# Optimization experiments

Hardware: AMD Instinct MI355X
Metric: run time of the kernel (lower is better)

Reference implementation:

```python
import jax, jax.numpy as jnp
import numpy as np

XS, YS = 512, 512  # xsize+1, ysize+1 with init args 511, 511


def _grid_sample_align_corners(img, gx, gy):
    """Bilinear grid_sample with align_corners=True, zeros padding.
    img: [C, H, W]; gx, gy: [X, Y] normalized coords in grid_sample convention
    (gx indexes W, gy indexes H). Returns [C, X, Y]."""
    C, H, W = img.shape
    x = (gx + 1.0) * 0.5 * (W - 1)
    y = (gy + 1.0) * 0.5 * (H - 1)
    x0 = jnp.floor(x)
    y0 = jnp.floor(y)
    wx1 = x - x0
    wy1 = y - y0
    out = jnp.zeros((C,) + gx.shape, img.dtype)
    for dy in (0, 1):
        for dx in (0, 1):
            xi = x0 + dx
            yi = y0 + dy
            w = (wx1 if dx else 1.0 - wx1) * (wy1 if dy else 1.0 - wy1)
            valid = (xi >= 0) & (xi <= W - 1) & (yi >= 0) & (yi <= H - 1)
            xc = jnp.clip(xi, 0, W - 1).astype(jnp.int32)
            yc = jnp.clip(yi, 0, H - 1).astype(jnp.int32)
            v = img[:, yc, xc]  # [C, X, Y]
            out = out + v * (w * valid.astype(img.dtype))[None]
    return out


def _per_batch(a, b, c, pnts, coors, contain):
    # a/b/c: [C,H,W] feature maps; pnts: [P,2] in [0,1]; coors: [P,3] int; contain: [P] int
    keep = contain > 0
    # route invalid pillars to an out-of-bounds index -> dropped by scatter
    cx = jnp.where(keep, coors[:, 1], XS)
    cy = jnp.where(keep, coors[:, 2], YS)
    grid = jnp.full((XS, YS, 2), -2.0, a.dtype)
    grid = grid.at[cx, cy, :].set(pnts * 2.0 - 1.0, mode='drop')
    mask = jnp.zeros((XS, YS), a.dtype).at[cx, cy].set(1.0, mode='drop')
    gx, gy = grid[..., 0], grid[..., 1]
    fa = _grid_sample_align_corners(a, gx, gy) * mask[None]
    fb = _grid_sample_align_corners(b, gx, gy) * mask[None]
    fc = _grid_sample_align_corners(c, gx, gy) * mask[None]
    return fa, fb, fc


def reference(c3, c4, c5, dynamic_img, pillar_img_pts, rgb_coors, contains_rgb):
    fa, fb, fc = jax.vmap(_per_batch)(c3, c4, c5, pillar_img_pts, rgb_coors, contains_rgb)
    # weighted fusion of the three scales, weights broadcast over channel dim
    return (fa * dynamic_img[:, 0:1]
            + fb * dynamic_img[:, 1:2]
            + fc * dynamic_img[:, 2:3])


def setup_inputs() -> dict:
    key = jax.random.key(0)
    ks = jax.random.split(key, 7)
    B, C, P = 4, 64, 20000
    c3 = jax.random.normal(ks[0], (B, C, 48, 160), jnp.float32)
    c4 = jax.random.normal(ks[1], (B, C, 24, 80), jnp.float32)
    c5 = jax.random.normal(ks[2], (B, C, 12, 40), jnp.float32)
    dynamic_img = jax.random.uniform(ks[3], (B, 3, XS, YS), jnp.float32)
    pillar_img_pts = jax.random.uniform(ks[4], (B, P, 2), jnp.float32)
    rgb_coors = jax.random.randint(ks[5], (B, P, 3), 0, 512, jnp.int32)
    contains_rgb = jax.random.randint(ks[6], (B, P), 0, 2, jnp.int32)
    return {"c3": c3, "c4": c4, "c5": c5, "dynamic_img": dynamic_img,
            "pillar_img_pts": pillar_img_pts, "rgb_coors": rgb_coors,
            "contains_rgb": contains_rgb}
```

## Files before the change

### kernel.cpp

```cpp
#include <hip/hip_runtime.h>
#include <cstddef>

#define XSZ 512
#define YSZ 512
#define NB  4
#define NC  64
#define NP  20000
#define H3 48
#define W3 160
#define H4 24
#define W4 80
#define H5 12
#define W5 40
#define HW3 (H3*W3)
#define HW4 (H4*W4)
#define HW5 (H5*W5)

#define FILL_BLOCKS 256
#define T3_TILES (NB * ((HW3 + 63) / 64))
#define T4_TILES (NB * ((HW4 + 63) / 64))
#define T5_TILES (NB * ((HW5 + 63) / 64))

__global__ void __launch_bounds__(256)
k_init(int4* __restrict__ winner4,
       const float* __restrict__ c3, const float* __restrict__ c4,
       const float* __restrict__ c5,
       float* __restrict__ c3t, float* __restrict__ c4t, float* __restrict__ c5t) {
    int blk = blockIdx.x;
    if (blk < FILL_BLOCKS) {
        int base = blk * 1024 + threadIdx.x;
        int4 m1 = make_int4(-1, -1, -1, -1);
        winner4[base      ] = m1;
        winner4[base + 256] = m1;
        winner4[base + 512] = m1;
        winner4[base + 768] = m1;
        return;
    }
    __shared__ float lds[NC * 65];
    int t = blk - FILL_BLOCKS;
    const float* in; float* outp; int HW, tpb;
    if (t < T3_TILES)                      { in = c3; outp = c3t; HW = HW3; tpb = 120; }
    else if ((t -= T3_TILES) < T4_TILES)   { in = c4; outp = c4t; HW = HW4; tpb = 30; }
    else { t -= T4_TILES;                    in = c5; outp = c5t; HW = HW5; tpb = 8; }
    int b  = t / tpb;
    int p0 = (t - b * tpb) * 64;
    int lane = threadIdx.x & 63, wave = threadIdx.x >> 6;
    const float* in_b  = in   + (size_t)b * NC * HW;
    float*       out_b = outp + (size_t)b * HW * NC;

    int p = p0 + lane;
    if (p < HW) {
        for (int ch = wave; ch < NC; ch += 4)
            lds[ch * 65 + lane] = in_b[(size_t)ch * HW + p];
    }
    __syncthreads();
    for (int pp = wave; pp < 64; pp += 4) {
        int pq = p0 + pp;
        if (pq < HW) out_b[(size_t)pq * NC + lane] = lds[lane * 65 + pp];
    }
}

__global__ void __launch_bounds__(256)
k_scatter(const int* __restrict__ coors, const int* __restrict__ contains,
          int* __restrict__ winner) {
    int idx = blockIdx.x * blockDim.x + threadIdx.x;
    if (idx >= NB * NP) return;
    if (contains[idx] <= 0) return;
    int b  = idx / NP;
    int p  = idx - b * NP;
    int cx = coors[idx * 3 + 1];
    int cy = coors[idx * 3 + 2];
    if ((unsigned)cx >= XSZ || (unsigned)cy >= YSZ) return;
    atomicMax(&winner[((size_t)b * XSZ + cx) * YSZ + cy], p);
}

__device__ __forceinline__ float bilinT(const float* __restrict__ img, int H, int W,
                                        float px, float py, int c) {
    float gx = px * 2.0f - 1.0f;
    float gy = py * 2.0f - 1.0f;
    float x = (gx + 1.0f) * 0.5f * (float)(W - 1);
    float y = (gy + 1.0f) * 0.5f * (float)(H - 1);
    float x0f = floorf(x), y0f = floorf(y);
    float wx1 = x - x0f,   wy1 = y - y0f;
    float wx0 = 1.0f - wx1, wy0 = 1.0f - wy1;
    int x0 = (int)x0f, y0 = (int)y0f;
    float acc = 0.0f;
#pragma unroll
    for (int dy = 0; dy < 2; ++dy) {
#pragma unroll
        for (int dx = 0; dx < 2; ++dx) {
            int xi = x0 + dx, yi = y0 + dy;
            bool valid = (xi >= 0) && (xi <= W - 1) && (yi >= 0) && (yi <= H - 1);
            int xc = min(max(xi, 0), W - 1);
            int yc = min(max(yi, 0), H - 1);
            float w = (dx ? wx1 : wx0) * (dy ? wy1 : wy0);
            float v = img[(size_t)(yc * W + xc) * NC + c];
            acc = fmaf(v, valid ? w : 0.0f, acc);
        }
    }
    return acc;
}

__device__ __forceinline__ float bilinG(const float* __restrict__ img, int H, int W,
                                        float px, float py, int c, int sChan) {
    float gx = px * 2.0f - 1.0f;
    float gy = py * 2.0f - 1.0f;
    float x = (gx + 1.0f) * 0.5f * (float)(W - 1);
    float y = (gy + 1.0f) * 0.5f * (float)(H - 1);
    float x0f = floorf(x), y0f = floorf(y);
    float wx1 = x - x0f,   wy1 = y - y0f;
    float wx0 = 1.0f - wx1, wy0 = 1.0f - wy1;
    int x0 = (int)x0f, y0 = (int)y0f;
    float acc = 0.0f;
#pragma unroll
    for (int dy = 0; dy < 2; ++dy) {
#pragma unroll
        for (int dx = 0; dx < 2; ++dx) {
            int xi = x0 + dx, yi = y0 + dy;
            bool valid = (xi >= 0) && (xi <= W - 1) && (yi >= 0) && (yi <= H - 1);
            int xc = min(max(xi, 0), W - 1);
            int yc = min(max(yi, 0), H - 1);
            float w = (dx ? wx1 : wx0) * (dy ? wy1 : wy0);
            float v = img[(size_t)(yc * W + xc) + (size_t)c * sChan];
            acc = fmaf(v, valid ? w : 0.0f, acc);
        }
    }
    return acc;
}

__global__ void __launch_bounds__(256)
k_samp(const int* __restrict__ coors, const int* __restrict__ contains,
       const float* __restrict__ pnts, const int* __restrict__ winner,
       const float* __restrict__ i3t, const float* __restrict__ i4t,
       const float* __restrict__ i5t, const float* __restrict__ dyn,
       float* __restrict__ cvals) {
    int nw   = gridDim.x << 2;
    int wv   = (blockIdx.x << 2) + (threadIdx.x >> 6);
    int lane = threadIdx.x & 63;
    for (int idx = wv; idx < NB * NP; idx += nw) {
        if (contains[idx] <= 0) continue;
        int b = idx / NP;
        int p = idx - b * NP;
        int cx = coors[idx * 3 + 1];
        int cy = coors[idx * 3 + 2];
        if ((unsigned)cx >= XSZ || (unsigned)cy >= YSZ) continue;
        if (winner[((size_t)b * XSZ + cx) * YSZ + cy] != p) continue;
        float px = pnts[idx * 2], py = pnts[idx * 2 + 1];
        float fa = bilinT(i3t + (size_t)b * HW3 * NC, H3, W3, px, py, lane);
        float fb = bilinT(i4t + (size_t)b * HW4 * NC, H4, W4, px, py, lane);
        float fc = bilinT(i5t + (size_t)b * HW5 * NC, H5, W5, px, py, lane);
        size_t dbase = (((size_t)b * 3) * XSZ + cx) * YSZ + cy;
        float d0 = dyn[dbase];
        float d1 = dyn[dbase + (size_t)XSZ * YSZ];
        float d2 = dyn[dbase + (size_t)2 * XSZ * YSZ];
        cvals[(size_t)idx * NC + lane] = fa * d0 + fb * d1 + fc * d2;
    }
}

__global__ void __launch_bounds__(256)
k_samp_fb(const int* __restrict__ coors, const int* __restrict__ contains,
          const float* __restrict__ pnts, const int* __restrict__ winner,
          const float* __restrict__ i3, const float* __restrict__ i4,
          const float* __restrict__ i5, const float* __restrict__ dyn,
          float* __restrict__ out) {
    int nw   = gridDim.x << 2;
    int wv   = (blockIdx.x << 2) + (threadIdx.x >> 6);
    int lane = threadIdx.x & 63;
    for (int idx = wv; idx < NB * NP; idx += nw) {
        if (contains[idx] <= 0) continue;
        int b = idx / NP;
        int p = idx - b * NP;
        int cx = coors[idx * 3 + 1];
        int cy = coors[idx * 3 + 2];
        if ((unsigned)cx >= XSZ || (unsigned)cy >= YSZ) continue;
        if (winner[((size_t)b * XSZ + cx) * YSZ + cy] != p) continue;
        float px = pnts[idx * 2], py = pnts[idx * 2 + 1];
        float fa = bilinG(i3 + (size_t)b * NC * HW3, H3, W3, px, py, lane, HW3);
        float fb = bilinG(i4 + (size_t)b * NC * HW4, H4, W4, px, py, lane, HW4);
        float fc = bilinG(i5 + (size_t)b * NC * HW5, H5, W5, px, py, lane, HW5);
        size_t dbase = (((size_t)b * 3) * XSZ + cx) * YSZ + cy;
        float d0 = dyn[dbase];
        float d1 = dyn[dbase + (size_t)XSZ * YSZ];
        float d2 = dyn[dbase + (size_t)2 * XSZ * YSZ];
        out[(((size_t)b * NC + lane) * XSZ + cx) * YSZ + cy] = fa * d0 + fb * d1 + fc * d2;
    }
}

__global__ void __launch_bounds__(256)
k_writeout(const int* __restrict__ winner, const float* __restrict__ cvals,
           float* __restrict__ out) {
    int bx = blockIdx.x;
    int b = bx >> 9, x = bx & 511;
    const int4* wrow = (const int4*)(winner + ((size_t)b * XSZ + x) * YSZ);
    int4 r = wrow[threadIdx.x & 127];
    int lane_c = threadIdx.x >> 7;
    int y4 = (threadIdx.x & 127) << 2;
    size_t obase = (size_t)b * NC * XSZ * YSZ + (size_t)x * YSZ + y4;
    size_t pb = (size_t)b * NP;

    bool h0 = r.x >= 0, h1 = r.y >= 0, h2 = r.z >= 0, h3 = r.w >= 0;
    size_t s0 = (pb + (unsigned)r.x) * NC;
    size_t s1 = (pb + (unsigned)r.y) * NC;
    size_t s2 = (pb + (unsigned)r.z) * NC;
    size_t s3 = (pb + (unsigned)r.w) * NC;

    for (int cb = 0; cb < NC; cb += 2) {
        int c = cb + lane_c;
        float4 v = make_float4(0.f, 0.f, 0.f, 0.f);
        if (h0) v.x = cvals[s0 + c];
        if (h1) v.y = cvals[s1 + c];
        if (h2) v.z = cvals[s2 + c];
        if (h3) v.w = cvals[s3 + c];
        *(float4*)(out + obase + (size_t)c * (XSZ * YSZ)) = v;
    }
}

__global__ void k_zero4(float4* __restrict__ p, long n4) {
    long i = (long)blockIdx.x * blockDim.x + threadIdx.x;
    long stride = (long)gridDim.x * blockDim.x;
    for (; i < n4; i += stride) p[i] = make_float4(0.f, 0.f, 0.f, 0.f);
}

extern "C" void kernel_launch(void* const* d_in, const int* in_sizes, int n_in,
                              void* d_out, int out_size, void* d_ws, size_t ws_size,
                              hipStream_t stream) {
    const float* c3       = (const float*)d_in[0];
    const float* c4       = (const float*)d_in[1];
    const float* c5       = (const float*)d_in[2];
    const float* dyn      = (const float*)d_in[3];
    const float* pnts     = (const float*)d_in[4];
    const int*   coors    = (const int*)d_in[5];
    const int*   contains = (const int*)d_in[6];
    float* out = (float*)d_out;

    char* ws = (char*)d_ws;
    size_t off = 0;
    int* winner = (int*)(ws + off);   off += (size_t)NB * XSZ * YSZ * 4;
    float* c3t  = (float*)(ws + off); off += (size_t)NB * NC * HW3 * 4;
    float* c4t  = (float*)(ws + off); off += (size_t)NB * NC * HW4 * 4;
    float* c5t  = (float*)(ws + off); off += (size_t)NB * NC * HW5 * 4;
    size_t t_need = off;
    float* cvals = (float*)(ws + off); off += (size_t)NB * NP * NC * 4;
    size_t full_need = off;

    bool useT    = (ws_size >= t_need);
    bool useFull = (ws_size >= full_need);

    int npts = NB * NP;
    int init_blocks = useT ? (FILL_BLOCKS + T3_TILES + T4_TILES + T5_TILES)
                           : FILL_BLOCKS;
    k_init<<<init_blocks, 256, 0, stream>>>((int4*)winner, c3, c4, c5,
                                            c3t, c4t, c5t);
    k_scatter<<<(npts + 255) / 256, 256, 0, stream>>>(coors, contains, winner);

    if (useFull) {
        k_samp<<<2048, 256, 0, stream>>>(coors, contains, pnts, winner,
                                         c3t, c4t, c5t, dyn, cvals);
        k_writeout<<<NB * XSZ, 256, 0, stream>>>(winner, cvals, out);
    } else {
        long n4 = (long)out_size / 4;
        k_zero4<<<8192, 256, 0, stream>>>((float4*)out, n4);
        if (useT) {
            k_samp<<<2048, 256, 0, stream>>>(coors, contains, pnts, winner,
                                             c3t, c4t, c5t, dyn, nullptr);
            k_samp_fb<<<2048, 256, 0, stream>>>(coors, contains, pnts, winner,
                                                c3, c4, c5, dyn, out);
        } else {
            k_samp_fb<<<2048, 256, 0, stream>>>(coors, contains, pnts, winner,
                                                c3, c4, c5, dyn, out);
        }
    }
}
```

Measured before the change: 86.99 us.

## Fuse sampling and writeout into one per-row kernel with LDS staging

Replaces the two-kernel path (per-point sampling into a global cvals buffer, then a per-row writeout) with one kernel per (batch, x) row. Each block compacts that row's winner entries into an LDS slot list, computes the bilinear features for each occupied cell into LDS, and then writes the dense output row directly. This removes the global round trip through the 20 MB cvals buffer and one launch. In exchange, sampling work is now tied to row occupancy, and rows with more than 128 occupied cells take a slower overflow path that writes directly to global memory.

```diff
diff --git a/kernel.cpp b/kernel.cpp
--- a/kernel.cpp
+++ b/kernel.cpp
@@ -15,6 +15,7 @@
 #define HW3 (H3*W3)
 #define HW4 (H4*W4)
 #define HW5 (H5*W5)
+#define SLOT_CAP 128
 
 #define FILL_BLOCKS 256
 #define T3_TILES (NB * ((HW3 + 63) / 64))
@@ -129,31 +130,89 @@
 }
 
 __global__ void __launch_bounds__(256)
-k_samp(const int* __restrict__ coors, const int* __restrict__ contains,
-       const float* __restrict__ pnts, const int* __restrict__ winner,
-       const float* __restrict__ i3t, const float* __restrict__ i4t,
-       const float* __restrict__ i5t, const float* __restrict__ dyn,
-       float* __restrict__ cvals) {
-    int nw   = gridDim.x << 2;
-    int wv   = (blockIdx.x << 2) + (threadIdx.x >> 6);
-    int lane = threadIdx.x & 63;
-    for (int idx = wv; idx < NB * NP; idx += nw) {
-        if (contains[idx] <= 0) continue;
-        int b = idx / NP;
-        int p = idx - b * NP;
-        int cx = coors[idx * 3 + 1];
-        int cy = coors[idx * 3 + 2];
-        if ((unsigned)cx >= XSZ || (unsigned)cy >= YSZ) continue;
-        if (winner[((size_t)b * XSZ + cx) * YSZ + cy] != p) continue;
+k_fused(const float* __restrict__ pnts, const int* __restrict__ winner,
+        const float* __restrict__ i3t, const float* __restrict__ i4t,
+        const float* __restrict__ i5t, const float* __restrict__ dyn,
+        float* __restrict__ out) {
+    __shared__ float vec[SLOT_CAP * 65];
+    __shared__ int smap[YSZ];
+    __shared__ int slist[YSZ];
+    __shared__ int ylist[YSZ];
+    __shared__ int cnt;
+
+    int bx = blockIdx.x;
+    int b = bx >> 9, x = bx & 511;
+    int tid = threadIdx.x;
+    if (tid == 0) cnt = 0;
+    __syncthreads();
+
+    const int2* wrow2 = (const int2*)(winner + ((size_t)b * XSZ + x) * YSZ);
+    int2 r2 = wrow2[tid];
+    {
+        int y0 = tid * 2;
+        int pv0 = r2.x, pv1 = r2.y;
+        int s0 = -1, s1 = -1;
+        if (pv0 >= 0) { s0 = atomicAdd(&cnt, 1); slist[s0] = pv0; ylist[s0] = y0; }
+        if (pv1 >= 0) { s1 = atomicAdd(&cnt, 1); slist[s1] = pv1; ylist[s1] = y0 + 1; }
+        smap[y0]     = s0;
+        smap[y0 + 1] = s1;
+    }
+    __syncthreads();
+    int n = cnt;
+    int nB = min(n, SLOT_CAP);
+
+    int wave = tid >> 6, lane = tid & 63;
+    const float* i3b = i3t + (size_t)b * HW3 * NC;
+    const float* i4b = i4t + (size_t)b * HW4 * NC;
+    const float* i5b = i5t + (size_t)b * HW5 * NC;
+    for (int s = wave; s < nB; s += 4) {
+        int p = slist[s], y = ylist[s];
+        int idx = b * NP + p;
         float px = pnts[idx * 2], py = pnts[idx * 2 + 1];
-        float fa = bilinT(i3t + (size_t)b * HW3 * NC, H3, W3, px, py, lane);
-        float fb = bilinT(i4t + (size_t)b * HW4 * NC, H4, W4, px, py, lane);
-        float fc = bilinT(i5t + (size_t)b * HW5 * NC, H5, W5, px, py, lane);
-        size_t dbase = (((size_t)b * 3) * XSZ + cx) * YSZ + cy;
+        float fa = bilinT(i3b, H3, W3, px, py, lane);
+        float fb = bilinT(i4b, H4, W4, px, py, lane);
+        float fc = bilinT(i5b, H5, W5, px, py, lane);
+        size_t dbase = (((size_t)b * 3) * XSZ + x) * YSZ + y;
         float d0 = dyn[dbase];
         float d1 = dyn[dbase + (size_t)XSZ * YSZ];
         float d2 = dyn[dbase + (size_t)2 * XSZ * YSZ];
-        cvals[(size_t)idx * NC + lane] = fa * d0 + fb * d1 + fc * d2;
+        vec[s * 65 + lane] = fa * d0 + fb * d1 + fc * d2;
+    }
+    __syncthreads();
+
+    int lane_c = tid >> 7;
+    int t7 = tid & 127;
+    int y4 = t7 << 2;
+    int s0 = smap[y4], s1 = smap[y4 + 1], s2 = smap[y4 + 2], s3 = smap[y4 + 3];
+    bool h0 = (unsigned)s0 < SLOT_CAP, h1 = (unsigned)s1 < SLOT_CAP;
+    bool h2 = (unsigned)s2 < SLOT_CAP, h3 = (unsigned)s3 < SLOT_CAP;
+    size_t obase = (size_t)b * NC * XSZ * YSZ + (size_t)x * YSZ + y4;
+    for (int cb = 0; cb < NC; cb += 2) {
+        int c = cb + lane_c;
+        float4 v = make_float4(0.f, 0.f, 0.f, 0.f);
+        if (h0) v.x = vec[s0 * 65 + c];
+        if (h1) v.y = vec[s1 * 65 + c];
+        if (h2) v.z = vec[s2 * 65 + c];
+        if (h3) v.w = vec[s3 * 65 + c];
+        *(float4*)(out + obase + (size_t)c * (XSZ * YSZ)) = v;
+    }
+
+    if (n > SLOT_CAP) {
+        __syncthreads();
+        for (int s = SLOT_CAP + wave; s < n; s += 4) {
+            int p = slist[s], y = ylist[s];
+            int idx = b * NP + p;
+            float px = pnts[idx * 2], py = pnts[idx * 2 + 1];
+            float fa = bilinT(i3b, H3, W3, px, py, lane);
+            float fb = bilinT(i4b, H4, W4, px, py, lane);
+            float fc = bilinT(i5b, H5, W5, px, py, lane);
+            size_t dbase = (((size_t)b * 3) * XSZ + x) * YSZ + y;
+            float d0 = dyn[dbase];
+            float d1 = dyn[dbase + (size_t)XSZ * YSZ];
+            float d2 = dyn[dbase + (size_t)2 * XSZ * YSZ];
+            out[(((size_t)b * NC + lane) * XSZ + x) * YSZ + y] =
+                fa * d0 + fb * d1 + fc * d2;
+        }
     }
 }
 
@@ -186,35 +245,6 @@
     }
 }
 
-__global__ void __launch_bounds__(256)
-k_writeout(const int* __restrict__ winner, const float* __restrict__ cvals,
-           float* __restrict__ out) {
-    int bx = blockIdx.x;
-    int b = bx >> 9, x = bx & 511;
-    const int4* wrow = (const int4*)(winner + ((size_t)b * XSZ + x) * YSZ);
-    int4 r = wrow[threadIdx.x & 127];
-    int lane_c = threadIdx.x >> 7;
-    int y4 = (threadIdx.x & 127) << 2;
-    size_t obase = (size_t)b * NC * XSZ * YSZ + (size_t)x * YSZ + y4;
-    size_t pb = (size_t)b * NP;
-
-    bool h0 = r.x >= 0, h1 = r.y >= 0, h2 = r.z >= 0, h3 = r.w >= 0;
-    size_t s0 = (pb + (unsigned)r.x) * NC;
-    size_t s1 = (pb + (unsigned)r.y) * NC;
-    size_t s2 = (pb + (unsigned)r.z) * NC;
-    size_t s3 = (pb + (unsigned)r.w) * NC;
-
-    for (int cb = 0; cb < NC; cb += 2) {
-        int c = cb + lane_c;
-        float4 v = make_float4(0.f, 0.f, 0.f, 0.f);
-        if (h0) v.x = cvals[s0 + c];
-        if (h1) v.y = cvals[s1 + c];
-        if (h2) v.z = cvals[s2 + c];
-        if (h3) v.w = cvals[s3 + c];
-        *(float4*)(out + obase + (size_t)c * (XSZ * YSZ)) = v;
-    }
-}
-
 __global__ void k_zero4(float4* __restrict__ p, long n4) {
     long i = (long)blockIdx.x * blockDim.x + threadIdx.x;
     long stride = (long)gridDim.x * blockDim.x;
@@ -240,11 +270,7 @@
     float* c4t  = (float*)(ws + off); off += (size_t)NB * NC * HW4 * 4;
     float* c5t  = (float*)(ws + off); off += (size_t)NB * NC * HW5 * 4;
     size_t t_need = off;
-    float* cvals = (float*)(ws + off); off += (size_t)NB * NP * NC * 4;
-    size_t full_need = off;
-
-    bool useT    = (ws_size >= t_need);
-    bool useFull = (ws_size >= full_need);
+    bool useT = (ws_size >= t_need);
 
     int npts = NB * NP;
     int init_blocks = useT ? (FILL_BLOCKS + T3_TILES + T4_TILES + T5_TILES)
@@ -253,21 +279,13 @@
                                             c3t, c4t, c5t);
     k_scatter<<<(npts + 255) / 256, 256, 0, stream>>>(coors, contains, winner);
 
-    if (useFull) {
-        k_samp<<<2048, 256, 0, stream>>>(coors, contains, pnts, winner,
-                                         c3t, c4t, c5t, dyn, cvals);
-        k_writeout<<<NB * XSZ, 256, 0, stream>>>(winner, cvals, out);
+    if (useT) {
+        k_fused<<<NB * XSZ, 256, 0, stream>>>(pnts, winner, c3t, c4t, c5t,
+                                              dyn, out);
     } else {
         long n4 = (long)out_size / 4;
         k_zero4<<<8192, 256, 0, stream>>>((float4*)out, n4);
-        if (useT) {
-            k_samp<<<2048, 256, 0, stream>>>(coors, contains, pnts, winner,
-                                             c3t, c4t, c5t, dyn, nullptr);
-            k_samp_fb<<<2048, 256, 0, stream>>>(coors, contains, pnts, winner,
-                                                c3, c4, c5, dyn, out);
-        } else {
-            k_samp_fb<<<2048, 256, 0, stream>>>(coors, contains, pnts, winner,
-                                                c3, c4, c5, dyn, out);
-        }
-    }
-}
+        k_samp_fb<<<2048, 256, 0, stream>>>(coors, contains, pnts, winner,
+                                            c3, c4, c5, dyn, out);
+    }
+}
```

New measurement: 75.73 us. 12.9% less time.
